# Optimization experiments

Hardware: AMD Instinct MI355X
Metric: run time of the kernel (lower is better)

## Reference

```python
import math
import jax, jax.numpy as jnp
import numpy as np

B, N, L, D = 4, 16, 1024, 64  # batch, heads, seq len (L1=L2), head dim


def rel_shift(x):
    """Transformer-XL positional shift: [b,n,q,p]->[b,n,q,k] aligning relative positions."""
    b, n, q, k = x.shape
    x = jnp.pad(x, ((0, 0), (0, 0), (0, 0), (1, 0)))  # pad one zero column in front
    x = x.reshape(b, n, k + 1, q)
    return x[:, :, 1:, :].reshape(b, n, q, k)


def setup_inputs() -> dict:
    rng = jax.random.key(0)
    k1, k2, k3, k4, k5 = jax.random.split(rng, 5)
    query_content_biased = jax.random.normal(k1, (B, N, L, D), dtype=jnp.float32)
    query_pos_biased = jax.random.normal(k2, (B, N, L, D), dtype=jnp.float32)
    key = jax.random.normal(k3, (B, N, L, D), dtype=jnp.float32)
    value = jax.random.normal(k4, (B, N, L, D), dtype=jnp.float32)
    pos_encodings = jax.random.normal(k5, (N, L, D), dtype=jnp.float32)
    # causal mask: True = masked (as in torch masked_fill), broadcast over b,n
    mask = jnp.triu(jnp.ones((L, L), dtype=bool), k=1)[None, None]
    return {
        "query_content_biased": query_content_biased,
        "query_pos_biased": query_pos_biased,
        "key": key,
        "value": value,
        "pos_encodings": pos_encodings,
        "mask": mask,
    }


def reference(query_content_biased, query_pos_biased, key, value, pos_encodings, mask):
    # content scores: [b,n,i,j]
    weight = jnp.einsum('bnid,bnjd->bnij', query_content_biased, key)
    # positional scores, shifted into key axis
    pos_scores = jnp.einsum('bnid,npd->bnip', query_pos_biased, pos_encodings)
    weight = weight + rel_shift(pos_scores)
    weight = weight / math.sqrt(key.shape[-1])
    neg = jnp.finfo(weight.dtype).min
    weight = jnp.where(mask, neg, weight)
    weight = jax.nn.softmax(weight, axis=-1)
    weight = jnp.where(mask, jnp.zeros((), weight.dtype), weight)
    # dropout is identity at p=0.0 (eval)
    out = jnp.einsum('bnij,bnjd->bnid', weight, value)
    return (out, weight)
```

## Files before the change

### kernel.cpp

```cpp
#include <hip/hip_runtime.h>
#include <math.h>


#define Bq 4
#define Nh 16
#define Lq 1024
#define Dh 64
#define TQ 16
#define NT 256
#define LPAD 1028

typedef __attribute__((ext_vector_type(8))) short bf16x8;
typedef __attribute__((ext_vector_type(4))) float f32x4;

__device__ __forceinline__ unsigned short f2bf(float f) {
    union { float f; unsigned int u; } v; v.f = f;
    unsigned int u = v.u;
    unsigned int r = u + 0x7FFFu + ((u >> 16) & 1u);
    return (unsigned short)(r >> 16);
}

__device__ __forceinline__ bf16x8 ldg8(const unsigned short* p) {
    return *(const bf16x8*)p;
}

__device__ __forceinline__ float wave_max(float v) {
    #pragma unroll
    for (int o = 32; o > 0; o >>= 1) v = fmaxf(v, __shfl_xor(v, o));
    return v;
}
__device__ __forceinline__ float wave_sum(float v) {
    #pragma unroll
    for (int o = 32; o > 0; o >>= 1) v += __shfl_xor(v, o);
    return v;
}

__global__ __launch_bounds__(256) void cvt_bf16_kernel(
    const float* __restrict__ src, unsigned short* __restrict__ dst, int n4)
{
    int idx = blockIdx.x * 256 + threadIdx.x;
    if (idx >= n4) return;
    float4 v = ((const float4*)src)[idx];
    ushort4 o;
    o.x = f2bf(v.x); o.y = f2bf(v.y); o.z = f2bf(v.z); o.w = f2bf(v.w);
    ((ushort4*)dst)[idx] = o;
}

__global__ __launch_bounds__(256) void vt_kernel(
    const float* __restrict__ V, unsigned short* __restrict__ Vt)
{
    __shared__ float t[64][65];
    int bn = blockIdx.x >> 4, jt = blockIdx.x & 15;
    int tid = threadIdx.x;
    int d = tid & 63, q = tid >> 6;
    const float* vb = V + ((size_t)(bn * Lq + jt * 64)) * Dh;
    #pragma unroll
    for (int r = 0; r < 16; r++) {
        int jl = r * 4 + q;
        t[jl][d] = vb[(size_t)jl * Dh + d];
    }
    __syncthreads();
    int dd = tid >> 2, jb = (tid & 3) << 4;
    bf16x8 s0, s1;
    #pragma unroll
    for (int jj = 0; jj < 8; jj++) {
        s0[jj] = (short)f2bf(t[jb + jj][dd]);
        s1[jj] = (short)f2bf(t[jb + 8 + jj][dd]);
    }
    unsigned short* drow = Vt + (((size_t)(bn * 64 + dd)) << 10) + (jt << 6) + jb;
    *(bf16x8*)drow = s0;
    *(bf16x8*)(drow + 8) = s1;
}

__global__ __launch_bounds__(NT, 2) void relattn_kernel(
    const unsigned short* __restrict__ QCb, const unsigned short* __restrict__ QPb,
    const unsigned short* __restrict__ Kb,  const unsigned short* __restrict__ Pb,
    const unsigned short* __restrict__ Vtb,
    float* __restrict__ out, float* __restrict__ wout)
{
    __shared__ float s_s[TQ][LPAD];

    const int tid  = threadIdx.x;
    const int w    = tid >> 6, lane = tid & 63;
    const int ln   = lane & 15, quad = lane >> 4;
    const int bn   = blockIdx.x >> 6, qt = blockIdx.x & 63;
    const int nh   = bn & 15;
    const int i0   = qt << 4, i1 = i0 + 15;

    const unsigned short* qcrow = QCb + (((size_t)(bn << 10) + i0 + ln) << 6) + (quad << 3);
    const unsigned short* qprow = QPb + (((size_t)(bn << 10) + i0 + ln) << 6) + (quad << 3);
    bf16x8 aC0 = ldg8(qcrow), aC1 = ldg8(qcrow + 32);
    bf16x8 aP0 = ldg8(qprow), aP1 = ldg8(qprow + 32);

    const unsigned short* kbase = Kb + (((size_t)(bn << 10)) << 6) + (quad << 3);
    #pragma unroll
    for (int ct = 0; ct < 16; ct++) {
        int c0 = ((ct << 2) + w) << 4;
        if (c0 <= i1) {
            const unsigned short* kr = kbase + ((size_t)(c0 + ln) << 6);
            f32x4 acc = {0.f, 0.f, 0.f, 0.f};
            acc = __builtin_amdgcn_mfma_f32_16x16x32_bf16(aC0, ldg8(kr),      acc, 0, 0, 0);
            acc = __builtin_amdgcn_mfma_f32_16x16x32_bf16(aC1, ldg8(kr + 32), acc, 0, 0, 0);
            #pragma unroll
            for (int rg = 0; rg < 4; rg++)
                s_s[(quad << 2) + rg][c0 + ln] = acc[rg];
        }
    }
    __syncthreads();

    const unsigned short* pbase = Pb + (((size_t)(nh << 10)) << 6) + (quad << 3);
    #pragma unroll
    for (int ct = 0; ct < 16; ct++) {
        int p0 = ((ct << 2) + w) << 4;
        if (p0 + i0 + 30 >= 1023) {
            const unsigned short* pr = pbase + ((size_t)(p0 + ln) << 6);
            f32x4 acc = {0.f, 0.f, 0.f, 0.f};
            acc = __builtin_amdgcn_mfma_f32_16x16x32_bf16(aP0, ldg8(pr),      acc, 0, 0, 0);
            acc = __builtin_amdgcn_mfma_f32_16x16x32_bf16(aP1, ldg8(pr + 32), acc, 0, 0, 0);
            int p = p0 + ln;
            #pragma unroll
            for (int rg = 0; rg < 4; rg++) {
                int row = (quad << 2) + rg;
                int j = p + i0 + row - 1023;
                if (j >= 0) s_s[row][j] += acc[rg];
            }
        }
    }
    __syncthreads();

    #pragma unroll
    for (int rr = 0; rr < 4; rr++) {
        int r = (w << 2) + rr;
        int i = i0 + r;
        float mx = -3.0e38f;
        #pragma unroll
        for (int c = 0; c < 4; c++) {
            int j = (c << 8) + (lane << 2);
            float4 v = *(float4*)&s_s[r][j];
            if (j     <= i) mx = fmaxf(mx, v.x);
            if (j + 1 <= i) mx = fmaxf(mx, v.y);
            if (j + 2 <= i) mx = fmaxf(mx, v.z);
            if (j + 3 <= i) mx = fmaxf(mx, v.w);
        }
        mx = wave_max(mx);
        float sum = 0.f;
        #pragma unroll
        for (int c = 0; c < 4; c++) {
            int j = (c << 8) + (lane << 2);
            float4 v = *(float4*)&s_s[r][j];
            float4 e;
            e.x = (j     <= i) ? __expf((v.x - mx) * 0.125f) : 0.f;
            e.y = (j + 1 <= i) ? __expf((v.y - mx) * 0.125f) : 0.f;
            e.z = (j + 2 <= i) ? __expf((v.z - mx) * 0.125f) : 0.f;
            e.w = (j + 3 <= i) ? __expf((v.w - mx) * 0.125f) : 0.f;
            sum += e.x + e.y + e.z + e.w;
            *(float4*)&s_s[r][j] = e;
        }
        sum = wave_sum(sum);
        float inv = 1.0f / sum;
        float* wrow = wout + (((size_t)(bn << 10) + i) << 10);
        #pragma unroll
        for (int c = 0; c < 4; c++) {
            int j = (c << 8) + (lane << 2);
            float4 e = *(float4*)&s_s[r][j];
            e.x *= inv; e.y *= inv; e.z *= inv; e.w *= inv;
            *(float4*)&s_s[r][j] = e;
            *(float4*)&wrow[j]   = e;
        }
    }
    __syncthreads();

    f32x4 o = {0.f, 0.f, 0.f, 0.f};
    const int n0 = w << 4;
    const unsigned short* vtb = Vtb + (((size_t)(bn << 6) + n0 + ln) << 10);
    const int ksteps = (i0 + 16 + 31) >> 5;
    for (int ks = 0; ks < ksteps; ks++) {
        int k0 = (ks << 5) + (quad << 3);
        float4 a0 = *(float4*)&s_s[ln][k0];
        float4 a1 = *(float4*)&s_s[ln][k0 + 4];
        bf16x8 af;
        af[0] = (short)f2bf(a0.x); af[1] = (short)f2bf(a0.y);
        af[2] = (short)f2bf(a0.z); af[3] = (short)f2bf(a0.w);
        af[4] = (short)f2bf(a1.x); af[5] = (short)f2bf(a1.y);
        af[6] = (short)f2bf(a1.z); af[7] = (short)f2bf(a1.w);
        bf16x8 vb = ldg8(vtb + k0);
        o = __builtin_amdgcn_mfma_f32_16x16x32_bf16(af, vb, o, 0, 0, 0);
    }
    float* obase = out + (((size_t)(bn << 10) + i0) << 6);
    #pragma unroll
    for (int rg = 0; rg < 4; rg++)
        obase[((size_t)((quad << 2) + rg) << 6) + n0 + ln] = o[rg];
}

extern "C" void kernel_launch(void* const* d_in, const int* in_sizes, int n_in,
                              void* d_out, int out_size, void* d_ws, size_t ws_size,
                              hipStream_t stream) {
    const float* qc = (const float*)d_in[0];
    const float* qp = (const float*)d_in[1];
    const float* K  = (const float*)d_in[2];
    const float* V  = (const float*)d_in[3];
    const float* P  = (const float*)d_in[4];

    float* out  = (float*)d_out;
    float* wout = out + (size_t)Bq * Nh * Lq * Dh;

    const size_t NQ = (size_t)Bq * Nh * Lq * Dh;
    const size_t NP = (size_t)Nh * Lq * Dh;
    unsigned short* QCb = (unsigned short*)d_ws;
    unsigned short* QPb = QCb + NQ;
    unsigned short* Kb  = QPb + NQ;
    unsigned short* Pb  = Kb  + NQ;
    unsigned short* Vtb = Pb  + NP;

    cvt_bf16_kernel<<<(NQ / 4 + 255) / 256, 256, 0, stream>>>(qc, QCb, (int)(NQ / 4));
    cvt_bf16_kernel<<<(NQ / 4 + 255) / 256, 256, 0, stream>>>(qp, QPb, (int)(NQ / 4));
    cvt_bf16_kernel<<<(NQ / 4 + 255) / 256, 256, 0, stream>>>(K,  Kb,  (int)(NQ / 4));
    cvt_bf16_kernel<<<(NP / 4 + 255) / 256, 256, 0, stream>>>(P,  Pb,  (int)(NP / 4));
    vt_kernel<<<Bq * Nh * 16, 256, 0, stream>>>(V, Vtb);

    relattn_kernel<<<Bq * Nh * (Lq / TQ), NT, 0, stream>>>(QCb, QPb, Kb, Pb, Vtb, out, wout);
}
```

Before: 499.6 us.

## Fuse Q conversion into attention kernel, merge K/P casts, cache softmax in registers

Q and QP are now read as fp32 directly inside the attention kernel and packed to bf16 there, which removes two separate conversion launches and their workspace round trips. The K and P conversions are merged into one launch. Softmax keeps each row's 16 values in registers instead of re-reading shared memory three times. The normalized probabilities are written to shared memory as bf16, so the PV MFMA loop loads its operand directly without converting inside the loop. This costs a few more registers per thread and leaves part of the shared buffer unused.

```diff
diff --git a/kernel.cpp b/kernel.cpp
--- a/kernel.cpp
+++ b/kernel.cpp
@@ -20,6 +20,15 @@
     return (unsigned short)(r >> 16);
 }
 
+__device__ __forceinline__ bf16x8 pack8(float4 a, float4 b) {
+    bf16x8 o;
+    o[0] = (short)f2bf(a.x); o[1] = (short)f2bf(a.y);
+    o[2] = (short)f2bf(a.z); o[3] = (short)f2bf(a.w);
+    o[4] = (short)f2bf(b.x); o[5] = (short)f2bf(b.y);
+    o[6] = (short)f2bf(b.z); o[7] = (short)f2bf(b.w);
+    return o;
+}
+
 __device__ __forceinline__ bf16x8 ldg8(const unsigned short* p) {
     return *(const bf16x8*)p;
 }
@@ -35,11 +44,14 @@
     return v;
 }
 
-__global__ __launch_bounds__(256) void cvt_bf16_kernel(
-    const float* __restrict__ src, unsigned short* __restrict__ dst, int n4)
+__global__ __launch_bounds__(256) void cvt_kp_kernel(
+    const float* __restrict__ K, const float* __restrict__ P,
+    unsigned short* __restrict__ Kb, unsigned short* __restrict__ Pb)
 {
-    int idx = blockIdx.x * 256 + threadIdx.x;
-    if (idx >= n4) return;
+    int b = blockIdx.x;
+    const float* src; unsigned short* dst; int idx;
+    if (b < 4096) { idx = b * 256 + threadIdx.x; src = K; dst = Kb; }
+    else          { idx = (b - 4096) * 256 + threadIdx.x; src = P; dst = Pb; }
     float4 v = ((const float4*)src)[idx];
     ushort4 o;
     o.x = f2bf(v.x); o.y = f2bf(v.y); o.z = f2bf(v.z); o.w = f2bf(v.w);
@@ -73,12 +85,12 @@
 }
 
 __global__ __launch_bounds__(NT, 2) void relattn_kernel(
-    const unsigned short* __restrict__ QCb, const unsigned short* __restrict__ QPb,
-    const unsigned short* __restrict__ Kb,  const unsigned short* __restrict__ Pb,
+    const float* __restrict__ QC, const float* __restrict__ QP,
+    const unsigned short* __restrict__ Kb, const unsigned short* __restrict__ Pb,
     const unsigned short* __restrict__ Vtb,
     float* __restrict__ out, float* __restrict__ wout)
 {
-    __shared__ float s_s[TQ][LPAD];
+    __shared__ __align__(16) float s_s[TQ][LPAD];
 
     const int tid  = threadIdx.x;
     const int w    = tid >> 6, lane = tid & 63;
@@ -87,10 +99,12 @@
     const int nh   = bn & 15;
     const int i0   = qt << 4, i1 = i0 + 15;
 
-    const unsigned short* qcrow = QCb + (((size_t)(bn << 10) + i0 + ln) << 6) + (quad << 3);
-    const unsigned short* qprow = QPb + (((size_t)(bn << 10) + i0 + ln) << 6) + (quad << 3);
-    bf16x8 aC0 = ldg8(qcrow), aC1 = ldg8(qcrow + 32);
-    bf16x8 aP0 = ldg8(qprow), aP1 = ldg8(qprow + 32);
+    const float* qcrow = QC + (((size_t)(bn << 10) + i0 + ln) << 6) + (quad << 3);
+    const float* qprow = QP + (((size_t)(bn << 10) + i0 + ln) << 6) + (quad << 3);
+    bf16x8 aC0 = pack8(*(const float4*)qcrow,        *(const float4*)(qcrow + 4));
+    bf16x8 aC1 = pack8(*(const float4*)(qcrow + 32), *(const float4*)(qcrow + 36));
+    bf16x8 aP0 = pack8(*(const float4*)qprow,        *(const float4*)(qprow + 4));
+    bf16x8 aP1 = pack8(*(const float4*)(qprow + 32), *(const float4*)(qprow + 36));
 
     const unsigned short* kbase = Kb + (((size_t)(bn << 10)) << 6) + (quad << 3);
     #pragma unroll
@@ -132,40 +146,47 @@
     for (int rr = 0; rr < 4; rr++) {
         int r = (w << 2) + rr;
         int i = i0 + r;
+        float v[16];
+        #pragma unroll
+        for (int c = 0; c < 4; c++) {
+            float4 t = *(float4*)&s_s[r][(c << 8) + (lane << 2)];
+            v[c * 4 + 0] = t.x; v[c * 4 + 1] = t.y;
+            v[c * 4 + 2] = t.z; v[c * 4 + 3] = t.w;
+        }
         float mx = -3.0e38f;
         #pragma unroll
         for (int c = 0; c < 4; c++) {
             int j = (c << 8) + (lane << 2);
-            float4 v = *(float4*)&s_s[r][j];
-            if (j     <= i) mx = fmaxf(mx, v.x);
-            if (j + 1 <= i) mx = fmaxf(mx, v.y);
-            if (j + 2 <= i) mx = fmaxf(mx, v.z);
-            if (j + 3 <= i) mx = fmaxf(mx, v.w);
+            #pragma unroll
+            for (int e = 0; e < 4; e++)
+                if (j + e <= i) mx = fmaxf(mx, v[c * 4 + e]);
         }
         mx = wave_max(mx);
         float sum = 0.f;
         #pragma unroll
         for (int c = 0; c < 4; c++) {
             int j = (c << 8) + (lane << 2);
-            float4 v = *(float4*)&s_s[r][j];
-            float4 e;
-            e.x = (j     <= i) ? __expf((v.x - mx) * 0.125f) : 0.f;
-            e.y = (j + 1 <= i) ? __expf((v.y - mx) * 0.125f) : 0.f;
-            e.z = (j + 2 <= i) ? __expf((v.z - mx) * 0.125f) : 0.f;
-            e.w = (j + 3 <= i) ? __expf((v.w - mx) * 0.125f) : 0.f;
-            sum += e.x + e.y + e.z + e.w;
-            *(float4*)&s_s[r][j] = e;
+            #pragma unroll
+            for (int e = 0; e < 4; e++) {
+                float t = (j + e <= i) ? __expf((v[c * 4 + e] - mx) * 0.125f) : 0.f;
+                sum += t;
+                v[c * 4 + e] = t;
+            }
         }
         sum = wave_sum(sum);
         float inv = 1.0f / sum;
         float* wrow = wout + (((size_t)(bn << 10) + i) << 10);
+        char*  brow = (char*)s_s + (size_t)r * (LPAD * 4);
         #pragma unroll
         for (int c = 0; c < 4; c++) {
             int j = (c << 8) + (lane << 2);
-            float4 e = *(float4*)&s_s[r][j];
-            e.x *= inv; e.y *= inv; e.z *= inv; e.w *= inv;
-            *(float4*)&s_s[r][j] = e;
-            *(float4*)&wrow[j]   = e;
+            float4 e;
+            e.x = v[c * 4 + 0] * inv; e.y = v[c * 4 + 1] * inv;
+            e.z = v[c * 4 + 2] * inv; e.w = v[c * 4 + 3] * inv;
+            *(float4*)&wrow[j] = e;
+            ushort4 h;
+            h.x = f2bf(e.x); h.y = f2bf(e.y); h.z = f2bf(e.z); h.w = f2bf(e.w);
+            *(ushort4*)(brow + (size_t)j * 2) = h;
         }
     }
     __syncthreads();
@@ -173,17 +194,12 @@
     f32x4 o = {0.f, 0.f, 0.f, 0.f};
     const int n0 = w << 4;
     const unsigned short* vtb = Vtb + (((size_t)(bn << 6) + n0 + ln) << 10);
+    const char* abase = (const char*)s_s + (size_t)ln * (LPAD * 4);
     const int ksteps = (i0 + 16 + 31) >> 5;
     for (int ks = 0; ks < ksteps; ks++) {
         int k0 = (ks << 5) + (quad << 3);
-        float4 a0 = *(float4*)&s_s[ln][k0];
-        float4 a1 = *(float4*)&s_s[ln][k0 + 4];
-        bf16x8 af;
-        af[0] = (short)f2bf(a0.x); af[1] = (short)f2bf(a0.y);
-        af[2] = (short)f2bf(a0.z); af[3] = (short)f2bf(a0.w);
-        af[4] = (short)f2bf(a1.x); af[5] = (short)f2bf(a1.y);
-        af[6] = (short)f2bf(a1.z); af[7] = (short)f2bf(a1.w);
-        bf16x8 vb = ldg8(vtb + k0);
+        bf16x8 af = *(const bf16x8*)(abase + (size_t)k0 * 2);
+        bf16x8 vb = ldg8(vtb + (ks << 5) + (quad << 3));
         o = __builtin_amdgcn_mfma_f32_16x16x32_bf16(af, vb, o, 0, 0, 0);
     }
     float* obase = out + (((size_t)(bn << 10) + i0) << 6);
@@ -206,17 +222,11 @@
 
     const size_t NQ = (size_t)Bq * Nh * Lq * Dh;
     const size_t NP = (size_t)Nh * Lq * Dh;
-    unsigned short* QCb = (unsigned short*)d_ws;
-    unsigned short* QPb = QCb + NQ;
-    unsigned short* Kb  = QPb + NQ;
-    unsigned short* Pb  = Kb  + NQ;
-    unsigned short* Vtb = Pb  + NP;
-
-    cvt_bf16_kernel<<<(NQ / 4 + 255) / 256, 256, 0, stream>>>(qc, QCb, (int)(NQ / 4));
-    cvt_bf16_kernel<<<(NQ / 4 + 255) / 256, 256, 0, stream>>>(qp, QPb, (int)(NQ / 4));
-    cvt_bf16_kernel<<<(NQ / 4 + 255) / 256, 256, 0, stream>>>(K,  Kb,  (int)(NQ / 4));
-    cvt_bf16_kernel<<<(NP / 4 + 255) / 256, 256, 0, stream>>>(P,  Pb,  (int)(NP / 4));
+    unsigned short* Kb  = (unsigned short*)d_ws;
+    unsigned short* Pb  = Kb + NQ;
+    unsigned short* Vtb = Pb + NP;
+
+    cvt_kp_kernel<<<4096 + 1024, 256, 0, stream>>>(K, P, Kb, Pb);
     vt_kernel<<<Bq * Nh * 16, 256, 0, stream>>>(V, Vtb);
-
-    relattn_kernel<<<Bq * Nh * (Lq / TQ), NT, 0, stream>>>(QCb, QPb, Kb, Pb, Vtb, out, wout);
-}
+    relattn_kernel<<<Bq * Nh * (Lq / TQ), NT, 0, stream>>>(qc, qp, Kb, Pb, Vtb, out, wout);
+}
```

After: 488.9 us. -2.1%, faster.
